# Kernel optimization log

Measured on AMD Instinct MI355X. Metric: run time of the kernel, lower is better.

The kernel has to match this reference:

```python
import jax, jax.numpy as jnp
import numpy as np

NUM_BANDS = 64
LATENT = 256
HIDDEN = 512
G = 8
K = 1024
GD = LATENT // G  # 32
BETA = 0.25


def setup_inputs() -> dict:
    key = jax.random.key(0)
    ks = jax.random.split(key, 10)
    B, T = 16, 1000
    bands = jax.random.normal(ks[0], (B, T, NUM_BANDS), dtype=jnp.float32)
    s = 0.02
    enc_w1 = jax.random.normal(ks[1], (NUM_BANDS, HIDDEN), dtype=jnp.float32) * s
    enc_b1 = jnp.zeros((HIDDEN,), dtype=jnp.float32)
    enc_w2 = jax.random.normal(ks[2], (HIDDEN, LATENT), dtype=jnp.float32) * s
    enc_b2 = jnp.zeros((LATENT,), dtype=jnp.float32)
    codebooks = jax.random.normal(ks[3], (G, K, GD), dtype=jnp.float32) * 0.1
    dec_w1 = jax.random.normal(ks[4], (LATENT, HIDDEN), dtype=jnp.float32) * s
    dec_b1 = jnp.zeros((HIDDEN,), dtype=jnp.float32)
    dec_w2 = jax.random.normal(ks[5], (HIDDEN, NUM_BANDS), dtype=jnp.float32) * s
    dec_b2 = jnp.zeros((NUM_BANDS,), dtype=jnp.float32)
    return {
        "bands": bands,
        "enc_w1": enc_w1, "enc_b1": enc_b1, "enc_w2": enc_w2, "enc_b2": enc_b2,
        "codebooks": codebooks,
        "dec_w1": dec_w1, "dec_b1": dec_b1, "dec_w2": dec_w2, "dec_b2": dec_b2,
    }


def _mlp(x, w1, b1, w2, b2):
    # TimeDistributedMLP: Linear -> ReLU -> Linear applied on last dim
    return jax.nn.relu(x @ w1 + b1) @ w2 + b2


def reference(bands, enc_w1, enc_b1, enc_w2, enc_b2, codebooks,
              dec_w1, dec_b1, dec_w2, dec_b2):
    B, T, _ = bands.shape
    z_e = _mlp(bands, enc_w1, enc_b1, enc_w2, enc_b2)  # (B,T,LATENT)

    # Grouped VQ over flattened frames
    parts = z_e.reshape(B * T, G, GD)                   # (N,G,gd)
    zn = jnp.sum(parts * parts, axis=-1)[:, :, None]    # (N,G,1)
    cn = jnp.sum(codebooks * codebooks, axis=-1)[None]  # (1,G,K)
    cross = jnp.einsum('ngd,gkd->ngk', parts, codebooks)
    dist = zn - 2.0 * cross + cn                        # (N,G,K)
    idx = jnp.argmin(dist, axis=-1)                     # (N,G) int
    z_q = codebooks[jnp.arange(G)[None, :], idx]        # (N,G,gd) gather

    # straight-through estimator
    z_q_st = parts + jax.lax.stop_gradient(z_q - parts)

    # per-group mean losses, summed over groups
    codebook_loss = jnp.sum(jnp.mean((jax.lax.stop_gradient(z_q) - parts) ** 2, axis=(0, 2)))
    commit_loss = jnp.sum(jnp.mean((z_q - jax.lax.stop_gradient(parts)) ** 2, axis=(0, 2)))
    vq_loss = BETA * (codebook_loss + commit_loss)  # epoch=None -> beta_eff = beta

    z_q_out = z_q_st.reshape(B, T, LATENT)
    idx_out = idx.reshape(B, T, G)
    bands_hat = _mlp(z_q_out, dec_w1, dec_b1, dec_w2, dec_b2)
    return (bands_hat, z_e, z_q_out, idx_out, vq_loss)
```

## Files before the change

### kernel.cpp

```cpp
#include <hip/hip_runtime.h>

#define NBANDS 64
#define LATENT 256
#define HIDDEN 512
#define GQ 8
#define KQ 1024
#define GD 32
#define NROWS 16000

#define OUT_BH   0
#define OUT_ZE   1024000
#define OUT_ZQ   5120000
#define OUT_IDX  9216000
#define OUT_LOSS 9344000

#define WS_H     0
#define WS_H2BF_F  0
#define WS_ZQB_F   4096000
#define WS_W1B_F   6144000
#define WS_W2B_F   6209536
#define WS_CN    8192000
#define WS_LOSS  8200192

typedef __attribute__((ext_vector_type(8))) short bf16x8;
typedef __attribute__((ext_vector_type(4))) float f32x4;

__device__ __forceinline__ unsigned short f2bf(float f) {
  unsigned u = __builtin_bit_cast(unsigned, f);
  unsigned r = u + 0x7FFFu + ((u >> 16) & 1u);
  return (unsigned short)(r >> 16);
}

__device__ __forceinline__ void g2l16(const float* g, float* l) {
  __builtin_amdgcn_global_load_lds(
      (const __attribute__((address_space(1))) unsigned int*)g,
      (__attribute__((address_space(3))) unsigned int*)l, 16, 0, 0);
}

template<int BN, int TM, int TN, bool RELU>
__global__ __launch_bounds__(256) void gemm_f32(
    const float* __restrict__ A, const float* __restrict__ B,
    const float* __restrict__ bias, float* __restrict__ C,
    int M, int N, int K) {
  constexpr int BM = 128;
  constexpr int BK = 16;
  constexpr int NTX = BN / TN;

  __shared__ float As[BK][BM + 8];
  __shared__ float Bs[BK][BN + 4];

  const int tid = threadIdx.x;
  const int tx = tid % NTX;
  const int ty = tid / NTX;
  const int row0 = blockIdx.y * BM;
  const int col0 = blockIdx.x * BN;

  const int arow = tid >> 1;
  const int akq  = (tid & 1) * 8;
  const int bkk = tid >> 4;
  const int bn  = (tid & 15) * (BN / 16);

  float acc[TM][TN] = {};

  for (int k0 = 0; k0 < K; k0 += BK) {
    float4 av0 = *reinterpret_cast<const float4*>(
        &A[(size_t)(row0 + arow) * K + k0 + akq]);
    float4 av1 = *reinterpret_cast<const float4*>(
        &A[(size_t)(row0 + arow) * K + k0 + akq + 4]);
    float4 bv0, bv1;
    bv0 = *reinterpret_cast<const float4*>(
        &B[(size_t)(k0 + bkk) * N + col0 + bn]);
    if (BN == 128)
      bv1 = *reinterpret_cast<const float4*>(
          &B[(size_t)(k0 + bkk) * N + col0 + bn + 4]);
    __syncthreads();
    As[akq + 0][arow] = av0.x; As[akq + 1][arow] = av0.y;
    As[akq + 2][arow] = av0.z; As[akq + 3][arow] = av0.w;
    As[akq + 4][arow] = av1.x; As[akq + 5][arow] = av1.y;
    As[akq + 6][arow] = av1.z; As[akq + 7][arow] = av1.w;
    *reinterpret_cast<float4*>(&Bs[bkk][bn]) = bv0;
    if (BN == 128)
      *reinterpret_cast<float4*>(&Bs[bkk][bn + 4]) = bv1;
    __syncthreads();

#pragma unroll
    for (int kk = 0; kk < BK; ++kk) {
      float a[TM], b[TN];
#pragma unroll
      for (int q = 0; q < TM / 4; ++q) {
        float4 v = *reinterpret_cast<const float4*>(&As[kk][ty * TM + q * 4]);
        a[q * 4 + 0] = v.x; a[q * 4 + 1] = v.y;
        a[q * 4 + 2] = v.z; a[q * 4 + 3] = v.w;
      }
#pragma unroll
      for (int q = 0; q < TN / 4; ++q) {
        float4 v = *reinterpret_cast<const float4*>(&Bs[kk][tx * TN + q * 4]);
        b[q * 4 + 0] = v.x; b[q * 4 + 1] = v.y;
        b[q * 4 + 2] = v.z; b[q * 4 + 3] = v.w;
      }
#pragma unroll
      for (int i = 0; i < TM; ++i)
#pragma unroll
        for (int j = 0; j < TN; ++j)
          acc[i][j] = fmaf(a[i], b[j], acc[i][j]);
    }
  }

  float bb[TN];
#pragma unroll
  for (int q = 0; q < TN / 4; ++q) {
    float4 v = *reinterpret_cast<const float4*>(&bias[col0 + tx * TN + q * 4]);
    bb[q * 4 + 0] = v.x; bb[q * 4 + 1] = v.y;
    bb[q * 4 + 2] = v.z; bb[q * 4 + 3] = v.w;
  }
#pragma unroll
  for (int i = 0; i < TM; ++i) {
    const int r = row0 + ty * TM + i;
#pragma unroll
    for (int q = 0; q < TN / 4; ++q) {
      float4 v;
      float* vp = &v.x;
#pragma unroll
      for (int j = 0; j < 4; ++j) {
        float t = acc[i][q * 4 + j] + bb[q * 4 + j];
        if (RELU) t = fmaxf(t, 0.0f);
        vp[j] = t;
      }
      *reinterpret_cast<float4*>(&C[(size_t)r * N + col0 + tx * TN + q * 4]) = v;
    }
  }
}

template<int WM, bool OUT_BF16>
__global__ __launch_bounds__(256) void gemm_bf16_mfma(
    const unsigned short* __restrict__ A, const unsigned short* __restrict__ B,
    const float* __restrict__ bias, void* __restrict__ Cout,
    int M, int N, int K) {
  constexpr int BM = 4 * WM;
  constexpr int MT = WM / 16;

  __shared__ unsigned short As[BM][40];
  __shared__ unsigned short Bs[64][40];

  const int tid  = threadIdx.x;
  const int wave = tid >> 6;
  const int lane = tid & 63;
  const int quad = lane >> 4;
  const int l16  = lane & 15;
  const int row0 = blockIdx.y * BM;
  const int col0 = blockIdx.x * 64;

  f32x4 acc[MT][4];
#pragma unroll
  for (int mt = 0; mt < MT; ++mt)
#pragma unroll
    for (int nt = 0; nt < 4; ++nt) acc[mt][nt] = (f32x4){0.f, 0.f, 0.f, 0.f};

  for (int k0 = 0; k0 < K; k0 += 32) {
    __syncthreads();
    if constexpr (BM == 128) {
      const int r = tid >> 1, seg = (tid & 1) * 16;
      const uint4* src = reinterpret_cast<const uint4*>(
          &A[(size_t)(row0 + r) * K + k0 + seg]);
      uint4* dst = reinterpret_cast<uint4*>(&As[r][seg]);
      dst[0] = src[0]; dst[1] = src[1];
    } else {
      const int r = tid >> 2, seg = (tid & 3) * 8;
      *reinterpret_cast<uint4*>(&As[r][seg]) =
          *reinterpret_cast<const uint4*>(&A[(size_t)(row0 + r) * K + k0 + seg]);
    }
    {
      const int kk = tid >> 3, n0 = (tid & 7) * 8;
      uint4 bv = *reinterpret_cast<const uint4*>(
          &B[(size_t)(k0 + kk) * N + col0 + n0]);
      unsigned short t[8];
      *reinterpret_cast<uint4*>(t) = bv;
#pragma unroll
      for (int j = 0; j < 8; ++j) Bs[n0 + j][kk] = t[j];
    }
    __syncthreads();

    bf16x8 af[MT], bf[4];
#pragma unroll
    for (int mt = 0; mt < MT; ++mt)
      af[mt] = *reinterpret_cast<const bf16x8*>(
          &As[wave * WM + mt * 16 + l16][quad * 8]);
#pragma unroll
    for (int nt = 0; nt < 4; ++nt)
      bf[nt] = *reinterpret_cast<const bf16x8*>(&Bs[nt * 16 + l16][quad * 8]);
#pragma unroll
    for (int mt = 0; mt < MT; ++mt)
#pragma unroll
      for (int nt = 0; nt < 4; ++nt)
        acc[mt][nt] = __builtin_amdgcn_mfma_f32_16x16x32_bf16(
            af[mt], bf[nt], acc[mt][nt], 0, 0, 0);
  }

#pragma unroll
  for (int mt = 0; mt < MT; ++mt)
#pragma unroll
    for (int nt = 0; nt < 4; ++nt) {
      const int col = col0 + nt * 16 + l16;
      const float bv = bias[col];
#pragma unroll
      for (int r = 0; r < 4; ++r) {
        const int grow = row0 + wave * WM + mt * 16 + quad * 4 + r;
        float v = acc[mt][nt][r] + bv;
        if constexpr (OUT_BF16) {
          v = fmaxf(v, 0.0f);
          ((unsigned short*)Cout)[(size_t)grow * N + col] = f2bf(v);
        } else {
          ((float*)Cout)[(size_t)grow * N + col] = v;
        }
      }
    }
}

__global__ void cn_kernel(const float* __restrict__ cb, float* __restrict__ cn,
                          float* __restrict__ loss_acc) {
  const int i = blockIdx.x * 256 + threadIdx.x;
  if (i == 0) loss_acc[0] = 0.0f;
  if (i < GQ * KQ) {
    const float* c = cb + (size_t)i * GD;
    float s = 0.0f;
#pragma unroll
    for (int d = 0; d < GD; ++d) s = fmaf(c[d], c[d], s);
    cn[i] = s;
  }
}

__global__ void wconv_kernel(const float* __restrict__ w1, const float* __restrict__ w2,
                             unsigned short* __restrict__ w1b,
                             unsigned short* __restrict__ w2b) {
  const int i = blockIdx.x * 256 + threadIdx.x;
  const int n1 = LATENT * HIDDEN;
  const int n2 = HIDDEN * NBANDS;
  if (i < n1) w1b[i] = f2bf(w1[i]);
  else if (i < n1 + n2) w2b[i - n1] = f2bf(w2[i - n1]);
}

#define VQ_ROWS 128
#define VQ_CHUNK 128
#define VQ_NCHUNK (KQ / VQ_CHUNK)
#define ZPAD 36

__global__ __launch_bounds__(256) void vq_kernel(
    const float* __restrict__ z_e, const float* __restrict__ cb,
    const float* __restrict__ cn, float* __restrict__ z_q,
    unsigned short* __restrict__ zqb,
    float* __restrict__ idx_out, float* __restrict__ loss_acc) {
  const int g    = blockIdx.y;
  const int row0 = blockIdx.x * VQ_ROWS;
  const int tid  = threadIdx.x;
  const int tx   = tid & 15;
  const int ty   = tid >> 4;

  __shared__ float smem[VQ_ROWS * ZPAD + 2 * VQ_CHUNK * GD];
  float* zs  = smem;
  float* cbF = smem + VQ_ROWS * ZPAD;

  const float* cbg = cb + (size_t)g * KQ * GD;
  const float* cng = cn + (size_t)g * KQ;

  {
    const float* src = cbg;
    float* dst = cbF;
#pragma unroll
    for (int q4 = 0; q4 < 4; ++q4) {
      const int s = q4 * 256 + tid;
      const int r = s >> 3;
      const int q = (s & 7) ^ (r & 7);
      g2l16(src + r * GD + q * 4, dst + s * 4);
    }
  }

  {
    const int r   = tid >> 1;
    const int off = (tid & 1) << 4;
    const int key = ((r >> 3) & 3) << 2;
    const float4* src = reinterpret_cast<const float4*>(
        &z_e[(size_t)(row0 + r) * LATENT + g * GD + off]);
#pragma unroll
    for (int q = 0; q < 4; ++q)
      *reinterpret_cast<float4*>(&zs[r * ZPAD + ((off + q * 4) ^ key)]) = src[q];
  }

  const int akey = (ty & 3) << 2;
  const int bkey = tx & 7;

  float best[8];
  int   bidx[8];
#pragma unroll
  for (int i = 0; i < 8; ++i) { best[i] = 3.0e38f; bidx[i] = 0; }

  for (int ch = 0; ch < VQ_NCHUNK; ++ch) {
    __syncthreads();

    if (ch + 1 < VQ_NCHUNK) {
      const float* src = cbg + (size_t)(ch + 1) * VQ_CHUNK * GD;
      float* dst = cbF + ((ch + 1) & 1) * (VQ_CHUNK * GD);
#pragma unroll
      for (int q4 = 0; q4 < 4; ++q4) {
        const int s = q4 * 256 + tid;
        const int r = s >> 3;
        const int q = (s & 7) ^ (r & 7);
        g2l16(src + r * GD + q * 4, dst + s * 4);
      }
    }

    const float* cbuf = cbF + (ch & 1) * (VQ_CHUNK * GD);

    float acc[8][8];
#pragma unroll
    for (int i = 0; i < 8; ++i)
#pragma unroll
      for (int j = 0; j < 8; ++j) acc[i][j] = 0.0f;

#pragma unroll 2
    for (int d0 = 0; d0 < GD; d0 += 4) {
      float4 a[8], b[8];
#pragma unroll
      for (int s = 0; s < 8; ++s)
        a[s] = *reinterpret_cast<const float4*>(
            &zs[(ty * 8 + s) * ZPAD + (d0 ^ akey)]);
      const int bq = ((d0 >> 2) ^ bkey) << 2;
#pragma unroll
      for (int j = 0; j < 8; ++j)
        b[j] = *reinterpret_cast<const float4*>(
            &cbuf[(j * 16 + tx) * GD + bq]);
#pragma unroll
      for (int i = 0; i < 8; ++i)
#pragma unroll
        for (int j = 0; j < 8; ++j) {
          float t = acc[i][j];
          t = fmaf(a[i].x, b[j].x, t);
          t = fmaf(a[i].y, b[j].y, t);
          t = fmaf(a[i].z, b[j].z, t);
          t = fmaf(a[i].w, b[j].w, t);
          acc[i][j] = t;
        }
    }

#pragma unroll
    for (int j = 0; j < 8; ++j) {
      const int k = ch * VQ_CHUNK + j * 16 + tx;
      const float cnv = cng[k];
#pragma unroll
      for (int i = 0; i < 8; ++i) {
        const float dist = fmaf(-2.0f, acc[i][j], cnv);
        if (dist < best[i]) { best[i] = dist; bidx[i] = k; }
      }
    }
  }

  __syncthreads();
  float* m_d = cbF;
  int*   m_i = reinterpret_cast<int*>(cbF + 16 * 129);
  float* red = cbF + 2 * 16 * 129 + 32;
#pragma unroll
  for (int i = 0; i < 8; ++i) {
    m_d[tx * 129 + ty * 8 + i] = best[i];
    m_i[tx * 129 + ty * 8 + i] = bidx[i];
  }
  __syncthreads();

  float sse_part = 0.0f;
  if (tid < VQ_ROWS) {
    const int row = tid;
    const int rkey = ((row >> 3) & 3) << 2;
    float mb = m_d[row];
    int   mi = m_i[row];
#pragma unroll
    for (int t = 1; t < 16; ++t) {
      const float v = m_d[t * 129 + row];
      const int  ix = m_i[t * 129 + row];
      if (v < mb || (v == mb && ix < mi)) { mb = v; mi = ix; }
    }

    const float* c = cbg + (size_t)mi * GD;
    float cw[GD];
#pragma unroll
    for (int q = 0; q < 8; ++q) {
      float4 v = *reinterpret_cast<const float4*>(&c[q * 4]);
      cw[q * 4 + 0] = v.x; cw[q * 4 + 1] = v.y;
      cw[q * 4 + 2] = v.z; cw[q * 4 + 3] = v.w;
    }
    float sse = 0.0f;
#pragma unroll
    for (int d = 0; d < GD; ++d) {
      const float diff = cw[d] - zs[row * ZPAD + (d ^ rkey)];
      sse = fmaf(diff, diff, sse);
    }
    float4* zq = reinterpret_cast<float4*>(
        &z_q[(size_t)(row0 + row) * LATENT + g * GD]);
#pragma unroll
    for (int q = 0; q < 8; ++q)
      zq[q] = make_float4(cw[q * 4], cw[q * 4 + 1], cw[q * 4 + 2], cw[q * 4 + 3]);

    alignas(16) unsigned short zb[GD];
#pragma unroll
    for (int d = 0; d < GD; ++d) zb[d] = f2bf(cw[d]);
    uint4* dstb = reinterpret_cast<uint4*>(
        zqb + (size_t)(row0 + row) * LATENT + g * GD);
    const uint4* srcb = reinterpret_cast<const uint4*>(zb);
#pragma unroll
    for (int q = 0; q < 4; ++q) dstb[q] = srcb[q];

    idx_out[(size_t)(row0 + row) * GQ + g] = (float)mi;
    sse_part = sse;
  }

  if (tid < VQ_ROWS) red[tid] = sse_part;
  __syncthreads();
  if (tid < 64) {
    float s = red[tid] + red[tid + 64];
#pragma unroll
    for (int off = 32; off > 0; off >>= 1)
      s += __shfl_down(s, off, 64);
    if (tid == 0) atomicAdd(loss_acc, s);
  }
}

__global__ void loss_kernel(const float* __restrict__ acc,
                            float* __restrict__ out) {
  out[0] = 0.5f * acc[0] / (float)((size_t)NROWS * GD);
}

extern "C" void kernel_launch(void* const* d_in, const int* in_sizes, int n_in,
                              void* d_out, int out_size, void* d_ws, size_t ws_size,
                              hipStream_t stream) {
  const float* bands  = (const float*)d_in[0];
  const float* enc_w1 = (const float*)d_in[1];
  const float* enc_b1 = (const float*)d_in[2];
  const float* enc_w2 = (const float*)d_in[3];
  const float* enc_b2 = (const float*)d_in[4];
  const float* cbooks = (const float*)d_in[5];
  const float* dec_w1 = (const float*)d_in[6];
  const float* dec_b1 = (const float*)d_in[7];
  const float* dec_w2 = (const float*)d_in[8];
  const float* dec_b2 = (const float*)d_in[9];

  float* out = (float*)d_out;
  float* ws  = (float*)d_ws;

  float* bands_hat = out + OUT_BH;
  float* z_e       = out + OUT_ZE;
  float* z_q       = out + OUT_ZQ;
  float* idx_f     = out + OUT_IDX;
  float* loss_out  = out + OUT_LOSS;

  float* H        = ws + WS_H;
  float* cn       = ws + WS_CN;
  float* loss_acc = ws + WS_LOSS;
  unsigned short* h2bf = (unsigned short*)(ws + WS_H2BF_F);
  unsigned short* zqb  = (unsigned short*)(ws + WS_ZQB_F);
  unsigned short* w1b  = (unsigned short*)(ws + WS_W1B_F);
  unsigned short* w2b  = (unsigned short*)(ws + WS_W2B_F);

  cn_kernel<<<dim3((GQ * KQ + 255) / 256), dim3(256), 0, stream>>>(cbooks, cn, loss_acc);

  gemm_f32<128, 8, 8, true ><<<dim3(HIDDEN / 128, NROWS / 128), dim3(256), 0, stream>>>(
      bands, enc_w1, enc_b1, H, NROWS, HIDDEN, NBANDS);
  gemm_f32<64, 4, 8, false><<<dim3(LATENT / 64, NROWS / 128), dim3(256), 0, stream>>>(
      H, enc_w2, enc_b2, z_e, NROWS, LATENT, HIDDEN);

  wconv_kernel<<<dim3((LATENT * HIDDEN + HIDDEN * NBANDS + 255) / 256), dim3(256), 0, stream>>>(
      dec_w1, dec_w2, w1b, w2b);

  vq_kernel<<<dim3(NROWS / VQ_ROWS, GQ), dim3(256), 0, stream>>>(
      z_e, cbooks, cn, z_q, zqb, idx_f, loss_acc);

  gemm_bf16_mfma<32, true ><<<dim3(HIDDEN / 64, NROWS / 128), dim3(256), 0, stream>>>(
      zqb, w1b, dec_b1, (void*)h2bf, NROWS, HIDDEN, LATENT);
  gemm_bf16_mfma<16, false><<<dim3(NBANDS / 64, NROWS / 64), dim3(256), 0, stream>>>(
      h2bf, w2b, dec_b2, (void*)bands_hat, NROWS, NBANDS, HIDDEN);

  loss_kernel<<<1, 1, 0, stream>>>(loss_acc, loss_out);
}
```

Baseline: 321.4 us.

## Pre-transpose decoder weights, widen encoder GEMM K-tile, fold loss into decoder GEMM

Decoder weights are converted to bf16 in a transposed (N-major) layout so the MFMA GEMM loads B tiles with vector stores instead of scalar transposing LDS writes. The second encoder FP32 GEMM now uses a K tile of 32 instead of 16, halving the number of barrier-separated tile loads at the cost of more LDS. The final loss kernel launch is removed and its scalar write is folded into the first decoder GEMM, saving one launch. The transposing prep kernel reads its input with strided accesses, but it is small.

After: 317.8 us. About the same (-1.1%).

```diff
diff --git a/kernel.cpp b/kernel.cpp
--- a/kernel.cpp
+++ b/kernel.cpp
@@ -37,14 +37,16 @@
       (__attribute__((address_space(3))) unsigned int*)l, 16, 0, 0);
 }
 
-template<int BN, int TM, int TN, bool RELU>
+template<int BN, int TM, int TN, int BK, bool RELU>
 __global__ __launch_bounds__(256) void gemm_f32(
     const float* __restrict__ A, const float* __restrict__ B,
     const float* __restrict__ bias, float* __restrict__ C,
     int M, int N, int K) {
   constexpr int BM = 128;
-  constexpr int BK = 16;
   constexpr int NTX = BN / TN;
+  constexpr int AF4 = BK / 8;
+  constexpr int QPR = BN / 4;
+  constexpr int BF4 = BK * BN / 1024;
 
   __shared__ float As[BK][BM + 8];
   __shared__ float Bs[BK][BN + 4];
@@ -56,31 +58,37 @@
   const int col0 = blockIdx.x * BN;
 
   const int arow = tid >> 1;
-  const int akq  = (tid & 1) * 8;
-  const int bkk = tid >> 4;
-  const int bn  = (tid & 15) * (BN / 16);
+  const int akq  = (tid & 1) * (BK / 2);
 
   float acc[TM][TN] = {};
 
   for (int k0 = 0; k0 < K; k0 += BK) {
-    float4 av0 = *reinterpret_cast<const float4*>(
-        &A[(size_t)(row0 + arow) * K + k0 + akq]);
-    float4 av1 = *reinterpret_cast<const float4*>(
-        &A[(size_t)(row0 + arow) * K + k0 + akq + 4]);
-    float4 bv0, bv1;
-    bv0 = *reinterpret_cast<const float4*>(
-        &B[(size_t)(k0 + bkk) * N + col0 + bn]);
-    if (BN == 128)
-      bv1 = *reinterpret_cast<const float4*>(
-          &B[(size_t)(k0 + bkk) * N + col0 + bn + 4]);
+    float4 av[AF4], bv[BF4];
+#pragma unroll
+    for (int q = 0; q < AF4; ++q)
+      av[q] = *reinterpret_cast<const float4*>(
+          &A[(size_t)(row0 + arow) * K + k0 + akq + q * 4]);
+#pragma unroll
+    for (int t = 0; t < BF4; ++t) {
+      const int qq = tid * BF4 + t;
+      const int bk = qq / QPR, bn4 = qq % QPR;
+      bv[t] = *reinterpret_cast<const float4*>(
+          &B[(size_t)(k0 + bk) * N + col0 + bn4 * 4]);
+    }
     __syncthreads();
-    As[akq + 0][arow] = av0.x; As[akq + 1][arow] = av0.y;
-    As[akq + 2][arow] = av0.z; As[akq + 3][arow] = av0.w;
-    As[akq + 4][arow] = av1.x; As[akq + 5][arow] = av1.y;
-    As[akq + 6][arow] = av1.z; As[akq + 7][arow] = av1.w;
-    *reinterpret_cast<float4*>(&Bs[bkk][bn]) = bv0;
-    if (BN == 128)
-      *reinterpret_cast<float4*>(&Bs[bkk][bn + 4]) = bv1;
+#pragma unroll
+    for (int q = 0; q < AF4; ++q) {
+      As[akq + q * 4 + 0][arow] = av[q].x;
+      As[akq + q * 4 + 1][arow] = av[q].y;
+      As[akq + q * 4 + 2][arow] = av[q].z;
+      As[akq + q * 4 + 3][arow] = av[q].w;
+    }
+#pragma unroll
+    for (int t = 0; t < BF4; ++t) {
+      const int qq = tid * BF4 + t;
+      const int bk = qq / QPR, bn4 = qq % QPR;
+      *reinterpret_cast<float4*>(&Bs[bk][bn4 * 4]) = bv[t];
+    }
     __syncthreads();
 
 #pragma unroll
@@ -131,11 +139,12 @@
   }
 }
 
-template<int WM, bool OUT_BF16>
+template<int WM, bool OUT_BF16, bool DO_LOSS>
 __global__ __launch_bounds__(256) void gemm_bf16_mfma(
-    const unsigned short* __restrict__ A, const unsigned short* __restrict__ B,
+    const unsigned short* __restrict__ A, const unsigned short* __restrict__ BT,
     const float* __restrict__ bias, void* __restrict__ Cout,
-    int M, int N, int K) {
+    int M, int N, int K,
+    const float* __restrict__ loss_acc, float* __restrict__ loss_out) {
   constexpr int BM = 4 * WM;
   constexpr int MT = WM / 16;
 
@@ -149,6 +158,9 @@
   const int l16  = lane & 15;
   const int row0 = blockIdx.y * BM;
   const int col0 = blockIdx.x * 64;
+
+  if (DO_LOSS && blockIdx.x == 0 && blockIdx.y == 0 && tid == 0)
+    loss_out[0] = 0.5f * loss_acc[0] / (float)((size_t)NROWS * GD);
 
   f32x4 acc[MT][4];
 #pragma unroll
@@ -170,13 +182,9 @@
           *reinterpret_cast<const uint4*>(&A[(size_t)(row0 + r) * K + k0 + seg]);
     }
     {
-      const int kk = tid >> 3, n0 = (tid & 7) * 8;
-      uint4 bv = *reinterpret_cast<const uint4*>(
-          &B[(size_t)(k0 + kk) * N + col0 + n0]);
-      unsigned short t[8];
-      *reinterpret_cast<uint4*>(t) = bv;
-#pragma unroll
-      for (int j = 0; j < 8; ++j) Bs[n0 + j][kk] = t[j];
+      const int n = tid >> 2, kc = (tid & 3) * 8;
+      *reinterpret_cast<uint4*>(&Bs[n][kc]) =
+          *reinterpret_cast<const uint4*>(&BT[(size_t)(col0 + n) * K + k0 + kc]);
     }
     __syncthreads();
 
@@ -216,8 +224,8 @@
     }
 }
 
-__global__ void cn_kernel(const float* __restrict__ cb, float* __restrict__ cn,
-                          float* __restrict__ loss_acc) {
+__global__ void prep_cn(const float* __restrict__ cb, float* __restrict__ cn,
+                        float* __restrict__ loss_acc) {
   const int i = blockIdx.x * 256 + threadIdx.x;
   if (i == 0) loss_acc[0] = 0.0f;
   if (i < GQ * KQ) {
@@ -229,14 +237,26 @@
   }
 }
 
-__global__ void wconv_kernel(const float* __restrict__ w1, const float* __restrict__ w2,
-                             unsigned short* __restrict__ w1b,
-                             unsigned short* __restrict__ w2b) {
-  const int i = blockIdx.x * 256 + threadIdx.x;
-  const int n1 = LATENT * HIDDEN;
-  const int n2 = HIDDEN * NBANDS;
-  if (i < n1) w1b[i] = f2bf(w1[i]);
-  else if (i < n1 + n2) w2b[i - n1] = f2bf(w2[i - n1]);
+__global__ void prep_wT(const float* __restrict__ w1, const float* __restrict__ w2,
+                        unsigned short* __restrict__ w1bT,
+                        unsigned short* __restrict__ w2bT) {
+  const int t = blockIdx.x * 256 + threadIdx.x;
+  if (t < 16384) {
+    const int n = t >> 5, k0 = (t & 31) * 8;
+    alignas(16) unsigned short o[8];
+#pragma unroll
+    for (int q = 0; q < 8; ++q) o[q] = f2bf(w1[(size_t)(k0 + q) * HIDDEN + n]);
+    *reinterpret_cast<uint4*>(&w1bT[(size_t)n * LATENT + k0]) =
+        *reinterpret_cast<const uint4*>(o);
+  } else if (t < 20480) {
+    const int u = t - 16384;
+    const int n = u >> 6, k0 = (u & 63) * 8;
+    alignas(16) unsigned short o[8];
+#pragma unroll
+    for (int q = 0; q < 8; ++q) o[q] = f2bf(w2[(size_t)(k0 + q) * NBANDS + n]);
+    *reinterpret_cast<uint4*>(&w2bT[(size_t)n * HIDDEN + k0]) =
+        *reinterpret_cast<const uint4*>(o);
+  }
 }
 
 #define VQ_ROWS 128
@@ -419,11 +439,6 @@
       s += __shfl_down(s, off, 64);
     if (tid == 0) atomicAdd(loss_acc, s);
   }
-}
-
-__global__ void loss_kernel(const float* __restrict__ acc,
-                            float* __restrict__ out) {
-  out[0] = 0.5f * acc[0] / (float)((size_t)NROWS * GD);
 }
 
 extern "C" void kernel_launch(void* const* d_in, const int* in_sizes, int n_in,
@@ -454,26 +469,23 @@
   float* loss_acc = ws + WS_LOSS;
   unsigned short* h2bf = (unsigned short*)(ws + WS_H2BF_F);
   unsigned short* zqb  = (unsigned short*)(ws + WS_ZQB_F);
-  unsigned short* w1b  = (unsigned short*)(ws + WS_W1B_F);
-  unsigned short* w2b  = (unsigned short*)(ws + WS_W2B_F);
-
-  cn_kernel<<<dim3((GQ * KQ + 255) / 256), dim3(256), 0, stream>>>(cbooks, cn, loss_acc);
-
-  gemm_f32<128, 8, 8, true ><<<dim3(HIDDEN / 128, NROWS / 128), dim3(256), 0, stream>>>(
+  unsigned short* w1bT = (unsigned short*)(ws + WS_W1B_F);
+  unsigned short* w2bT = (unsigned short*)(ws + WS_W2B_F);
+
+  prep_cn<<<dim3(32), dim3(256), 0, stream>>>(cbooks, cn, loss_acc);
+
+  gemm_f32<128, 8, 8, 16, true ><<<dim3(HIDDEN / 128, NROWS / 128), dim3(256), 0, stream>>>(
       bands, enc_w1, enc_b1, H, NROWS, HIDDEN, NBANDS);
-  gemm_f32<64, 4, 8, false><<<dim3(LATENT / 64, NROWS / 128), dim3(256), 0, stream>>>(
+  gemm_f32<64, 4, 8, 32, false><<<dim3(LATENT / 64, NROWS / 128), dim3(256), 0, stream>>>(
       H, enc_w2, enc_b2, z_e, NROWS, LATENT, HIDDEN);
 
-  wconv_kernel<<<dim3((LATENT * HIDDEN + HIDDEN * NBANDS + 255) / 256), dim3(256), 0, stream>>>(
-      dec_w1, dec_w2, w1b, w2b);
+  prep_wT<<<dim3(80), dim3(256), 0, stream>>>(dec_w1, dec_w2, w1bT, w2bT);
 
   vq_kernel<<<dim3(NROWS / VQ_ROWS, GQ), dim3(256), 0, stream>>>(
       z_e, cbooks, cn, z_q, zqb, idx_f, loss_acc);
 
-  gemm_bf16_mfma<32, true ><<<dim3(HIDDEN / 64, NROWS / 128), dim3(256), 0, stream>>>(
-      zqb, w1b, dec_b1, (void*)h2bf, NROWS, HIDDEN, LATENT);
-  gemm_bf16_mfma<16, false><<<dim3(NBANDS / 64, NROWS / 64), dim3(256), 0, stream>>>(
-      h2bf, w2b, dec_b2, (void*)bands_hat, NROWS, NBANDS, HIDDEN);
-
-  loss_kernel<<<1, 1, 0, stream>>>(loss_acc, loss_out);
-}
+  gemm_bf16_mfma<32, true, true ><<<dim3(HIDDEN / 64, NROWS / 128), dim3(256), 0, stream>>>(
+      zqb, w1bT, dec_b1, (void*)h2bf, NROWS, HIDDEN, LATENT, loss_acc, loss_out);
+  gemm_bf16_mfma<16, false, false><<<dim3(NBANDS / 64, NROWS / 64), dim3(256), 0, stream>>>(
+      h2bf, w2bT, dec_b2, (void*)bands_hat, NROWS, NBANDS, HIDDEN, loss_acc, loss_out);
+}
```
